# Optimization experiments

Hardware: AMD Instinct MI355X
Metric: run time of the kernel (lower is better)

Reference implementation:

```python
import jax, jax.numpy as jnp
import numpy as np

N = 50000      # nodes
E = 1600000    # edges (avg degree 32)
D_IN = 32
D_EF = 16
D_H = 64
D_MSG = 32
D_UP = 32


def setup_inputs() -> dict:
    key = jax.random.key(0)
    ks = jax.random.split(key, 10)
    s = 0.05
    return {
        "x": jax.random.normal(ks[0], (N, D_IN), dtype=jnp.float32),
        "degrees": jax.random.uniform(ks[1], (N, 1), dtype=jnp.float32),
        "edge_features": jax.random.normal(ks[2], (E, D_EF), dtype=jnp.float32),
        "W1m": jax.random.normal(ks[3], (2 * D_IN + D_EF, D_H), dtype=jnp.float32) * s,
        "b1m": jnp.zeros((D_H,), dtype=jnp.float32),
        "W2m": jax.random.normal(ks[4], (D_H, D_MSG), dtype=jnp.float32) * s,
        "b2m": jnp.zeros((D_MSG,), dtype=jnp.float32),
        "W1u": jax.random.normal(ks[5], (D_IN + D_MSG, D_H), dtype=jnp.float32) * s,
        "b1u": jnp.zeros((D_H,), dtype=jnp.float32),
        "W2u": jax.random.normal(ks[6], (D_H, D_UP), dtype=jnp.float32) * s,
        "b2u": jnp.zeros((D_UP,), dtype=jnp.float32),
        "edge_index": jax.random.randint(ks[7], (2, E), 0, N, dtype=jnp.int64),
    }


def mlp2(h, W1, b1, W2, b2):
    return jax.nn.relu(h @ W1 + b1) @ W2 + b2


def reference(x, degrees, edge_features, W1m, b1m, W2m, b2m, W1u, b1u, W2u, b2u, edge_index):
    # flow = 'source_to_target': select=1 -> i = targets = edge_index[1],
    # j = sources = edge_index[0]; sparse.sum over dim 0 aggregates per target.
    src = edge_index[0]
    dst = edge_index[1]
    x_i = x[dst]                                  # [E, D_IN] target features
    x_j = x[src]                                  # [E, D_IN] source features
    msg_in = jnp.concatenate([x_i, x_j, edge_features], axis=-1)  # [E, 2*D_IN+D_EF]
    msgs = mlp2(msg_in, W1m, b1m, W2m, b2m)       # [E, D_MSG]
    agg = jax.ops.segment_sum(msgs, dst, num_segments=x.shape[0])  # [N, D_MSG]
    upd_in = jnp.concatenate([x, agg], axis=-1)   # [N, D_IN+D_MSG]
    return mlp2(upd_in, W1u, b1u, W2u, b2u)       # [N, D_UP]
```

## Files before the change

### kernel.cpp

```cpp
#include <hip/hip_runtime.h>
#include <hip/hip_bf16.h>

#define D_IN  32
#define D_EF  16
#define D_H   64
#define D_MSG 32
#define D_UP  32

typedef __fp16 v2h __attribute__((ext_vector_type(2)));

__device__ __forceinline__ unsigned bf16pair(float a, float b) {
    unsigned ua = __float_as_uint(a);
    ua = (ua + 0x7fffu + ((ua >> 16) & 1u)) >> 16;
    unsigned ub = __float_as_uint(b);
    ub = (ub + 0x7fffu + ((ub >> 16) & 1u)) >> 16;
    return ua | (ub << 16);
}
__device__ __forceinline__ float bf_lo(unsigned u) { return __uint_as_float(u << 16); }
__device__ __forceinline__ float bf_hi(unsigned u) { return __uint_as_float(u & 0xffff0000u); }

__global__ __launch_bounds__(256) void prep_kernel(
    const float* __restrict__ x,
    const float* __restrict__ W1m,
    const float* __restrict__ b1m,
    const int*   __restrict__ ei,
    float* __restrict__ P1,
    unsigned short* __restrict__ P2b,
    int* __restrict__ deg,
    int* __restrict__ rank,
    v2h* __restrict__ W1Ep,
    int n_nodes, int n_edges, int NBn, int NBe)
{
    int b = blockIdx.x;

    if (b < NBn) {
        int i = b * 256 + threadIdx.x;
        if (i >= n_nodes) return;

        float xi[D_IN];
        const float4* xp = (const float4*)(x + (size_t)i * D_IN);
#pragma unroll
        for (int k4 = 0; k4 < D_IN / 4; ++k4) {
            float4 v = xp[k4];
            xi[4 * k4 + 0] = v.x; xi[4 * k4 + 1] = v.y;
            xi[4 * k4 + 2] = v.z; xi[4 * k4 + 3] = v.w;
        }
        {
            float acc[D_H];
#pragma unroll
            for (int j = 0; j < D_H; ++j) acc[j] = b1m[j];
            for (int k = 0; k < D_IN; ++k) {
                float xv = xi[k];
                const float* wr = W1m + (size_t)k * D_H;
#pragma unroll
                for (int j = 0; j < D_H; ++j) acc[j] += xv * wr[j];
            }
            float4* o = (float4*)(P1 + (size_t)i * D_H);
#pragma unroll
            for (int j4 = 0; j4 < D_H / 4; ++j4)
                o[j4] = make_float4(acc[4 * j4], acc[4 * j4 + 1],
                                    acc[4 * j4 + 2], acc[4 * j4 + 3]);
        }
        {
            float acc[D_H];
#pragma unroll
            for (int j = 0; j < D_H; ++j) acc[j] = 0.0f;
            for (int k = 0; k < D_IN; ++k) {
                float xv = xi[k];
                const float* wr = W1m + (size_t)(k + D_IN) * D_H;
#pragma unroll
                for (int j = 0; j < D_H; ++j) acc[j] += xv * wr[j];
            }
            uint4* o = (uint4*)(P2b + (size_t)i * D_H);
#pragma unroll
            for (int j8 = 0; j8 < D_H / 8; ++j8) {
                uint4 q;
                q.x = bf16pair(acc[8 * j8 + 0], acc[8 * j8 + 1]);
                q.y = bf16pair(acc[8 * j8 + 2], acc[8 * j8 + 3]);
                q.z = bf16pair(acc[8 * j8 + 4], acc[8 * j8 + 5]);
                q.w = bf16pair(acc[8 * j8 + 6], acc[8 * j8 + 7]);
                o[j8] = q;
            }
        }
    } else if (b < NBn + NBe) {
        int e = (b - NBn) * 256 + threadIdx.x;
        if (e < n_edges)
            rank[e] = atomicAdd(&deg[ei[n_edges + e]], 1);
    } else {
        int t = threadIdx.x;
        const float* W1E = W1m + (size_t)(2 * D_IN) * D_H;
        for (int idx = t; idx < 8 * D_H; idx += 256) {
            int kp = idx >> 6, c = idx & 63;
            W1Ep[idx] = __builtin_amdgcn_cvt_pkrtz(W1E[(2 * kp) * D_H + c],
                                                   W1E[(2 * kp + 1) * D_H + c]);
        }
    }
}

__global__ __launch_bounds__(256) void scan_partials_kernel(
    const int* __restrict__ deg, int* __restrict__ bsum, int n_nodes)
{
    int idx = blockIdx.x * 256 + threadIdx.x;
    int v = (idx < n_nodes) ? deg[idx] : 0;
#pragma unroll
    for (int o = 1; o < 64; o <<= 1) v += __shfl_xor(v, o, 64);
    __shared__ int ws[4];
    int lane = threadIdx.x & 63, w = threadIdx.x >> 6;
    if (lane == 0) ws[w] = v;
    __syncthreads();
    if (threadIdx.x == 0) bsum[blockIdx.x] = ws[0] + ws[1] + ws[2] + ws[3];
}

__global__ __launch_bounds__(256) void scan_blockoffs_kernel(
    const int* __restrict__ bsum, int* __restrict__ boffs, int nb)
{
    __shared__ int sdata[256];
    int t = threadIdx.x;
    sdata[t] = (t < nb) ? bsum[t] : 0;
    __syncthreads();
    for (int off = 1; off < 256; off <<= 1) {
        int u = (t >= off) ? sdata[t - off] : 0;
        __syncthreads();
        sdata[t] += u;
        __syncthreads();
    }
    if (t < nb) boffs[t] = (t > 0) ? sdata[t - 1] : 0;
}

__global__ __launch_bounds__(256) void scan_final_kernel(
    const int* __restrict__ deg, const int* __restrict__ boffs,
    int* __restrict__ offs, int n_nodes)
{
    __shared__ int sdata[256];
    int t = threadIdx.x;
    int idx = blockIdx.x * 256 + t;
    sdata[t] = (idx < n_nodes) ? deg[idx] : 0;
    __syncthreads();
    for (int off = 1; off < 256; off <<= 1) {
        int u = (t >= off) ? sdata[t - off] : 0;
        __syncthreads();
        sdata[t] += u;
        __syncthreads();
    }
    int excl = boffs[blockIdx.x] + ((t > 0) ? sdata[t - 1] : 0);
    if (idx < n_nodes) offs[idx] = excl;
}

__global__ __launch_bounds__(256) void scatter_kernel(
    const int* __restrict__ ei,
    const int* __restrict__ rank,
    const int* __restrict__ offs,
    int2* __restrict__ edges_sorted,
    int n_edges)
{
    int e = blockIdx.x * blockDim.x + threadIdx.x;
    if (e < n_edges) {
        int s = ei[e];
        int d = ei[n_edges + e];
        int pos = offs[d] + rank[e];
        edges_sorted[pos] = make_int2(e, s);
    }
}

__global__ __launch_bounds__(256, 6) void gather_kernel(
    const float* __restrict__ ef,
    const v2h*  __restrict__ W1Ep,
    const float* __restrict__ P1,
    const unsigned short* __restrict__ P2b,
    const int*  __restrict__ deg,
    const int*  __restrict__ offs,
    const int2* __restrict__ edges_sorted,
    float* __restrict__ hagg,
    int n_nodes)
{
    const int lane = threadIdx.x & 63;
    const int cg   = __builtin_amdgcn_readfirstlane((int)(threadIdx.x >> 6));
    const int g    = lane >> 4;
    const int t    = lane & 15;
    const int n    = blockIdx.x * 4 + g;
    if (n >= n_nodes) return;

    const int start = offs[n];
    const int end   = start + deg[n];

    float p1q[16];
    {
        const float4* pp = (const float4*)(P1 + (size_t)n * D_H + cg * 16);
#pragma unroll
        for (int q = 0; q < 4; ++q) {
            float4 v = pp[q];
            p1q[4 * q + 0] = v.x; p1q[4 * q + 1] = v.y;
            p1q[4 * q + 2] = v.z; p1q[4 * q + 3] = v.w;
        }
    }

    const v2h* wbase = W1Ep + 16 * cg;

    float hacc[16];
#pragma unroll
    for (int c = 0; c < 16; ++c) hacc[c] = 0.0f;

    for (int i = start + t; i < end; i += 16) {
        int2 es = edges_sorted[i];
        const float4* efp = (const float4*)(ef + (size_t)es.x * D_EF);
        float4 f0 = efp[0], f1 = efp[1], f2 = efp[2], f3 = efp[3];
        const uint4* p2u = (const uint4*)(P2b + (size_t)es.y * D_H + cg * 16);
        uint4 b0 = p2u[0], b1 = p2u[1];

        v2h efh[D_EF / 2];
        efh[0] = __builtin_amdgcn_cvt_pkrtz(f0.x, f0.y);
        efh[1] = __builtin_amdgcn_cvt_pkrtz(f0.z, f0.w);
        efh[2] = __builtin_amdgcn_cvt_pkrtz(f1.x, f1.y);
        efh[3] = __builtin_amdgcn_cvt_pkrtz(f1.z, f1.w);
        efh[4] = __builtin_amdgcn_cvt_pkrtz(f2.x, f2.y);
        efh[5] = __builtin_amdgcn_cvt_pkrtz(f2.z, f2.w);
        efh[6] = __builtin_amdgcn_cvt_pkrtz(f3.x, f3.y);
        efh[7] = __builtin_amdgcn_cvt_pkrtz(f3.z, f3.w);

#pragma unroll
        for (int jj = 0; jj < 2; ++jj) {
            uint4 b = jj ? b1 : b0;
            float h[8];
            h[0] = p1q[8 * jj + 0] + bf_lo(b.x);
            h[1] = p1q[8 * jj + 1] + bf_hi(b.x);
            h[2] = p1q[8 * jj + 2] + bf_lo(b.y);
            h[3] = p1q[8 * jj + 3] + bf_hi(b.y);
            h[4] = p1q[8 * jj + 4] + bf_lo(b.z);
            h[5] = p1q[8 * jj + 5] + bf_hi(b.z);
            h[6] = p1q[8 * jj + 6] + bf_lo(b.w);
            h[7] = p1q[8 * jj + 7] + bf_hi(b.w);

#pragma unroll
            for (int kp = 0; kp < D_EF / 2; ++kp) {
                const v2h* wr = wbase + kp * D_H + 8 * jj;
#pragma unroll
                for (int c8 = 0; c8 < 8; ++c8)
                    h[c8] = __builtin_amdgcn_fdot2(efh[kp], wr[c8], h[c8], false);
            }

#pragma unroll
            for (int c8 = 0; c8 < 8; ++c8) {
                float r = h[c8] > 0.0f ? h[c8] : 0.0f;
                hacc[8 * jj + c8] += r;
            }
        }
    }

    float r1[8];
    {
        const bool up = (t & 8) != 0;
#pragma unroll
        for (int c = 0; c < 8; ++c) {
            float lo = hacc[c]     + __shfl_xor(hacc[c],     8, 16);
            float hi = hacc[c + 8] + __shfl_xor(hacc[c + 8], 8, 16);
            r1[c] = up ? hi : lo;
        }
    }
    float r2[4];
    {
        const bool up = (t & 4) != 0;
#pragma unroll
        for (int c = 0; c < 4; ++c) {
            float lo = r1[c]     + __shfl_xor(r1[c],     4, 16);
            float hi = r1[c + 4] + __shfl_xor(r1[c + 4], 4, 16);
            r2[c] = up ? hi : lo;
        }
    }
    float r3[2];
    {
        const bool up = (t & 2) != 0;
#pragma unroll
        for (int c = 0; c < 2; ++c) {
            float lo = r2[c]     + __shfl_xor(r2[c],     2, 16);
            float hi = r2[c + 2] + __shfl_xor(r2[c + 2], 2, 16);
            r3[c] = up ? hi : lo;
        }
    }
    float r4;
    {
        const bool up = (t & 1) != 0;
        float lo = r3[0] + __shfl_xor(r3[0], 1, 16);
        float hi = r3[1] + __shfl_xor(r3[1], 1, 16);
        r4 = up ? hi : lo;
    }

    hagg[(size_t)n * D_H + cg * 16 + t] = r4;
}

__global__ __launch_bounds__(256) void node_upd_kernel(
    const float* __restrict__ x,
    const float* __restrict__ hagg,
    const int*   __restrict__ deg,
    const float* __restrict__ b2m,
    const float* __restrict__ W2m,
    const float* __restrict__ W1u,
    const float* __restrict__ b1u,
    const float* __restrict__ W2u,
    const float* __restrict__ b2u,
    float* __restrict__ out,
    int n_nodes)
{
    int i = blockIdx.x * blockDim.x + threadIdx.x;
    if (i >= n_nodes) return;

    float in[D_IN + D_MSG];
    const float4* xp = (const float4*)(x + (size_t)i * D_IN);
#pragma unroll
    for (int k4 = 0; k4 < D_IN / 4; ++k4) {
        float4 v = xp[k4];
        in[4 * k4 + 0] = v.x; in[4 * k4 + 1] = v.y;
        in[4 * k4 + 2] = v.z; in[4 * k4 + 3] = v.w;
    }

    float dc = (float)deg[i];
#pragma unroll
    for (int m = 0; m < D_MSG; ++m) in[D_IN + m] = dc * b2m[m];

    const float4* hp = (const float4*)(hagg + (size_t)i * D_H);
    for (int j4 = 0; j4 < D_H / 4; ++j4) {
        float4 v = hp[j4];
        const float* w0 = W2m + (size_t)(4 * j4 + 0) * D_MSG;
        const float* w1 = W2m + (size_t)(4 * j4 + 1) * D_MSG;
        const float* w2 = W2m + (size_t)(4 * j4 + 2) * D_MSG;
        const float* w3 = W2m + (size_t)(4 * j4 + 3) * D_MSG;
#pragma unroll
        for (int m = 0; m < D_MSG; ++m)
            in[D_IN + m] += v.x * w0[m] + v.y * w1[m] + v.z * w2[m] + v.w * w3[m];
    }

    float h[D_H];
#pragma unroll
    for (int j = 0; j < D_H; ++j) h[j] = b1u[j];
    for (int k = 0; k < D_IN + D_MSG; ++k) {
        float v = in[k];
        const float* wr = W1u + (size_t)k * D_H;
#pragma unroll
        for (int j = 0; j < D_H; ++j) h[j] += v * wr[j];
    }

    float o[D_UP];
#pragma unroll
    for (int m = 0; m < D_UP; ++m) o[m] = b2u[m];
    for (int j = 0; j < D_H; ++j) {
        float r = h[j] > 0.0f ? h[j] : 0.0f;
        const float* wr = W2u + (size_t)j * D_UP;
#pragma unroll
        for (int m = 0; m < D_UP; ++m) o[m] += r * wr[m];
    }

    float4* op = (float4*)(out + (size_t)i * D_UP);
#pragma unroll
    for (int m4 = 0; m4 < D_UP / 4; ++m4)
        op[m4] = make_float4(o[4 * m4], o[4 * m4 + 1], o[4 * m4 + 2], o[4 * m4 + 3]);
}

extern "C" void kernel_launch(void* const* d_in, const int* in_sizes, int n_in,
                              void* d_out, int out_size, void* d_ws, size_t ws_size,
                              hipStream_t stream) {
    const float* x    = (const float*)d_in[0];
    const float* ef   = (const float*)d_in[2];
    const float* W1m  = (const float*)d_in[3];
    const float* b1m  = (const float*)d_in[4];
    const float* W2m  = (const float*)d_in[5];
    const float* b2m  = (const float*)d_in[6];
    const float* W1u  = (const float*)d_in[7];
    const float* b1u  = (const float*)d_in[8];
    const float* W2u  = (const float*)d_in[9];
    const float* b2u  = (const float*)d_in[10];
    const int*   ei   = (const int*)d_in[11];

    const int n_nodes = in_sizes[0] / D_IN;
    const int n_edges = in_sizes[11] / 2;

    float* out = (float*)d_out;

    const int NBn = (n_nodes + 255) / 256;
    const int NBe = (n_edges + 255) / 256;

    float*          P1  = (float*)d_ws;
    unsigned short* P2b = (unsigned short*)(P1 + (size_t)n_nodes * D_H);
    int2* edges_sorted  = (int2*)(P2b + (size_t)n_nodes * D_H);
    int* deg    = (int*)(edges_sorted + n_edges);
    int* offs   = deg    + n_nodes;
    int* bsum   = offs   + n_nodes;
    int* boffs  = bsum   + NBn;
    v2h* W1Ep   = (v2h*)(boffs + NBn);
    int*   rank = (int*)(W1Ep + 8 * D_H);
    float* hagg = (float*)rank;

    hipMemsetAsync(deg, 0, (size_t)n_nodes * sizeof(int), stream);

    prep_kernel<<<NBn + NBe + 1, 256, 0, stream>>>(
        x, W1m, b1m, ei, P1, P2b, deg, rank, W1Ep,
        n_nodes, n_edges, NBn, NBe);

    scan_partials_kernel<<<NBn, 256, 0, stream>>>(deg, bsum, n_nodes);
    scan_blockoffs_kernel<<<1, 256, 0, stream>>>(bsum, boffs, NBn);
    scan_final_kernel<<<NBn, 256, 0, stream>>>(deg, boffs, offs, n_nodes);

    scatter_kernel<<<NBe, 256, 0, stream>>>(ei, rank, offs, edges_sorted, n_edges);

    {
        int grid = (n_nodes + 3) / 4;
        gather_kernel<<<grid, 256, 0, stream>>>(ef, W1Ep, P1, P2b,
                                                deg, offs, edges_sorted, hagg,
                                                n_nodes);
    }
    node_upd_kernel<<<NBn, 256, 0, stream>>>(x, hagg, deg, b2m, W2m,
                                             W1u, b1u, W2u, b2u, out, n_nodes);
}
```

Before: 450.0 us.

## Fuse prep, scan and scatter into one cooperative kernel with register-held edges

Replaces the prep, three scan and scatter launches with a single cooperative persistent kernel that uses grid.sync between phases. Edge src, dst and rank are kept in registers (up to MAXE per thread) so the scatter phase does not re-read edge_index or a rank array, and the sorted edge list is written with nontemporal 64-bit stores. The gather loop is also unrolled to process two edges per iteration, giving more independent loads in flight. This trades launch overhead and memory round-trips for grid-wide barrier cost and register pressure, and it relies on the cooperative grid being large enough to cover NBn blocks.

```diff
diff --git a/kernel.cpp b/kernel.cpp
--- a/kernel.cpp
+++ b/kernel.cpp
@@ -1,11 +1,16 @@
 #include <hip/hip_runtime.h>
 #include <hip/hip_bf16.h>
+#include <hip/hip_cooperative_groups.h>
+
+namespace cg = cooperative_groups;
 
 #define D_IN  32
 #define D_EF  16
 #define D_H   64
 #define D_MSG 32
 #define D_UP  32
+
+#define MAXE 7
 
 typedef __fp16 v2h __attribute__((ext_vector_type(2)));
 
@@ -19,7 +24,7 @@
 __device__ __forceinline__ float bf_lo(unsigned u) { return __uint_as_float(u << 16); }
 __device__ __forceinline__ float bf_hi(unsigned u) { return __uint_as_float(u & 0xffff0000u); }
 
-__global__ __launch_bounds__(256) void prep_kernel(
+__global__ __launch_bounds__(256, 4) void front_kernel(
     const float* __restrict__ x,
     const float* __restrict__ W1m,
     const float* __restrict__ b1m,
@@ -27,16 +32,31 @@
     float* __restrict__ P1,
     unsigned short* __restrict__ P2b,
     int* __restrict__ deg,
-    int* __restrict__ rank,
+    int* __restrict__ offs,
+    int* __restrict__ bsum,
+    int* __restrict__ boffs,
     v2h* __restrict__ W1Ep,
-    int n_nodes, int n_edges, int NBn, int NBe)
+    long long* __restrict__ edges_sorted,
+    int* __restrict__ rank_ovf,
+    int n_nodes, int n_edges, int NBn)
 {
-    int b = blockIdx.x;
-
-    if (b < NBn) {
-        int i = b * 256 + threadIdx.x;
-        if (i >= n_nodes) return;
-
+    cg::grid_group grid = cg::this_grid();
+    const int t   = threadIdx.x;
+    const int tid = blockIdx.x * 256 + t;
+    const int nth = gridDim.x * 256;
+
+    __shared__ int sdata[256];
+
+    if (blockIdx.x == 0) {
+        const float* W1E = W1m + (size_t)(2 * D_IN) * D_H;
+        for (int idx = t; idx < 8 * D_H; idx += 256) {
+            int kp = idx >> 6, c = idx & 63;
+            W1Ep[idx] = __builtin_amdgcn_cvt_pkrtz(W1E[(2 * kp) * D_H + c],
+                                                   W1E[(2 * kp + 1) * D_H + c]);
+        }
+    }
+
+    for (int i = tid; i < n_nodes; i += nth) {
         float xi[D_IN];
         const float4* xp = (const float4*)(x + (size_t)i * D_IN);
 #pragma unroll
@@ -45,35 +65,35 @@
             xi[4 * k4 + 0] = v.x; xi[4 * k4 + 1] = v.y;
             xi[4 * k4 + 2] = v.z; xi[4 * k4 + 3] = v.w;
         }
-        {
-            float acc[D_H];
-#pragma unroll
-            for (int j = 0; j < D_H; ++j) acc[j] = b1m[j];
+        for (int half = 0; half < 2; ++half) {
+            float acc[32];
+#pragma unroll
+            for (int j = 0; j < 32; ++j) acc[j] = b1m[half * 32 + j];
             for (int k = 0; k < D_IN; ++k) {
                 float xv = xi[k];
-                const float* wr = W1m + (size_t)k * D_H;
-#pragma unroll
-                for (int j = 0; j < D_H; ++j) acc[j] += xv * wr[j];
-            }
-            float4* o = (float4*)(P1 + (size_t)i * D_H);
-#pragma unroll
-            for (int j4 = 0; j4 < D_H / 4; ++j4)
+                const float* wr = W1m + (size_t)k * D_H + half * 32;
+#pragma unroll
+                for (int j = 0; j < 32; ++j) acc[j] += xv * wr[j];
+            }
+            float4* o = (float4*)(P1 + (size_t)i * D_H + half * 32);
+#pragma unroll
+            for (int j4 = 0; j4 < 8; ++j4)
                 o[j4] = make_float4(acc[4 * j4], acc[4 * j4 + 1],
                                     acc[4 * j4 + 2], acc[4 * j4 + 3]);
         }
-        {
-            float acc[D_H];
-#pragma unroll
-            for (int j = 0; j < D_H; ++j) acc[j] = 0.0f;
+        for (int half = 0; half < 2; ++half) {
+            float acc[32];
+#pragma unroll
+            for (int j = 0; j < 32; ++j) acc[j] = 0.0f;
             for (int k = 0; k < D_IN; ++k) {
                 float xv = xi[k];
-                const float* wr = W1m + (size_t)(k + D_IN) * D_H;
-#pragma unroll
-                for (int j = 0; j < D_H; ++j) acc[j] += xv * wr[j];
-            }
-            uint4* o = (uint4*)(P2b + (size_t)i * D_H);
-#pragma unroll
-            for (int j8 = 0; j8 < D_H / 8; ++j8) {
+                const float* wr = W1m + (size_t)(k + D_IN) * D_H + half * 32;
+#pragma unroll
+                for (int j = 0; j < 32; ++j) acc[j] += xv * wr[j];
+            }
+            uint4* o = (uint4*)(P2b + (size_t)i * D_H + half * 32);
+#pragma unroll
+            for (int j8 = 0; j8 < 4; ++j8) {
                 uint4 q;
                 q.x = bf16pair(acc[8 * j8 + 0], acc[8 * j8 + 1]);
                 q.y = bf16pair(acc[8 * j8 + 2], acc[8 * j8 + 3]);
@@ -82,99 +102,97 @@
                 o[j8] = q;
             }
         }
-    } else if (b < NBn + NBe) {
-        int e = (b - NBn) * 256 + threadIdx.x;
-        if (e < n_edges)
-            rank[e] = atomicAdd(&deg[ei[n_edges + e]], 1);
-    } else {
-        int t = threadIdx.x;
-        const float* W1E = W1m + (size_t)(2 * D_IN) * D_H;
-        for (int idx = t; idx < 8 * D_H; idx += 256) {
-            int kp = idx >> 6, c = idx & 63;
-            W1Ep[idx] = __builtin_amdgcn_cvt_pkrtz(W1E[(2 * kp) * D_H + c],
-                                                   W1E[(2 * kp + 1) * D_H + c]);
-        }
-    }
-}
-
-__global__ __launch_bounds__(256) void scan_partials_kernel(
-    const int* __restrict__ deg, int* __restrict__ bsum, int n_nodes)
-{
-    int idx = blockIdx.x * 256 + threadIdx.x;
-    int v = (idx < n_nodes) ? deg[idx] : 0;
-#pragma unroll
-    for (int o = 1; o < 64; o <<= 1) v += __shfl_xor(v, o, 64);
-    __shared__ int ws[4];
-    int lane = threadIdx.x & 63, w = threadIdx.x >> 6;
-    if (lane == 0) ws[w] = v;
-    __syncthreads();
-    if (threadIdx.x == 0) bsum[blockIdx.x] = ws[0] + ws[1] + ws[2] + ws[3];
-}
-
-__global__ __launch_bounds__(256) void scan_blockoffs_kernel(
-    const int* __restrict__ bsum, int* __restrict__ boffs, int nb)
-{
-    __shared__ int sdata[256];
-    int t = threadIdx.x;
-    sdata[t] = (t < nb) ? bsum[t] : 0;
-    __syncthreads();
-    for (int off = 1; off < 256; off <<= 1) {
-        int u = (t >= off) ? sdata[t - off] : 0;
+    }
+
+    int esrc[MAXE], edst[MAXE], ernk[MAXE];
+#pragma unroll
+    for (int q = 0; q < MAXE; ++q) {
+        int e = tid + q * nth;
+        esrc[q] = 0; edst[q] = 0; ernk[q] = 0;
+        if (e < n_edges) {
+            esrc[q] = ei[e];
+            edst[q] = ei[n_edges + e];
+            ernk[q] = atomicAdd(&deg[edst[q]], 1);
+        }
+    }
+    for (int e = tid + MAXE * nth; e < n_edges; e += nth)
+        rank_ovf[e] = atomicAdd(&deg[ei[n_edges + e]], 1);
+
+    grid.sync();
+
+    {
+        int b = blockIdx.x;
+        if (b < NBn) {
+            int idx = b * 256 + t;
+            sdata[t] = (idx < n_nodes) ? deg[idx] : 0;
+            __syncthreads();
+            for (int off = 1; off < 256; off <<= 1) {
+                int u = (t >= off) ? sdata[t - off] : 0;
+                __syncthreads();
+                sdata[t] += u;
+                __syncthreads();
+            }
+            if (t == 255) bsum[b] = sdata[255];
+            if (idx < n_nodes) offs[idx] = (t > 0) ? sdata[t - 1] : 0;
+        }
+    }
+    grid.sync();
+
+    if (blockIdx.x == 0) {
+        sdata[t] = (t < NBn) ? bsum[t] : 0;
         __syncthreads();
-        sdata[t] += u;
-        __syncthreads();
-    }
-    if (t < nb) boffs[t] = (t > 0) ? sdata[t - 1] : 0;
-}
-
-__global__ __launch_bounds__(256) void scan_final_kernel(
-    const int* __restrict__ deg, const int* __restrict__ boffs,
-    int* __restrict__ offs, int n_nodes)
-{
-    __shared__ int sdata[256];
-    int t = threadIdx.x;
-    int idx = blockIdx.x * 256 + t;
-    sdata[t] = (idx < n_nodes) ? deg[idx] : 0;
-    __syncthreads();
-    for (int off = 1; off < 256; off <<= 1) {
-        int u = (t >= off) ? sdata[t - off] : 0;
-        __syncthreads();
-        sdata[t] += u;
-        __syncthreads();
-    }
-    int excl = boffs[blockIdx.x] + ((t > 0) ? sdata[t - 1] : 0);
-    if (idx < n_nodes) offs[idx] = excl;
-}
-
-__global__ __launch_bounds__(256) void scatter_kernel(
-    const int* __restrict__ ei,
-    const int* __restrict__ rank,
-    const int* __restrict__ offs,
-    int2* __restrict__ edges_sorted,
-    int n_edges)
-{
-    int e = blockIdx.x * blockDim.x + threadIdx.x;
-    if (e < n_edges) {
+        for (int off = 1; off < 256; off <<= 1) {
+            int u = (t >= off) ? sdata[t - off] : 0;
+            __syncthreads();
+            sdata[t] += u;
+            __syncthreads();
+        }
+        if (t < NBn) boffs[t] = (t > 0) ? sdata[t - 1] : 0;
+    }
+    grid.sync();
+
+    {
+        int b = blockIdx.x;
+        if (b > 0 && b < NBn) {
+            int idx = b * 256 + t;
+            if (idx < n_nodes) offs[idx] += boffs[b];
+        }
+    }
+    grid.sync();
+
+#pragma unroll
+    for (int q = 0; q < MAXE; ++q) {
+        int e = tid + q * nth;
+        if (e < n_edges) {
+            int pos = offs[edst[q]] + ernk[q];
+            long long v = (long long)((unsigned long long)(unsigned)esrc[q] << 32)
+                        | (unsigned long long)(unsigned)e;
+            __builtin_nontemporal_store(v, &edges_sorted[pos]);
+        }
+    }
+    for (int e = tid + MAXE * nth; e < n_edges; e += nth) {
         int s = ei[e];
         int d = ei[n_edges + e];
-        int pos = offs[d] + rank[e];
-        edges_sorted[pos] = make_int2(e, s);
+        int pos = offs[d] + rank_ovf[e];
+        long long v = (long long)((unsigned long long)(unsigned)s << 32)
+                    | (unsigned long long)(unsigned)e;
+        edges_sorted[pos] = v;
     }
 }
 
-__global__ __launch_bounds__(256, 6) void gather_kernel(
+__global__ __launch_bounds__(256) void gather_kernel(
     const float* __restrict__ ef,
     const v2h*  __restrict__ W1Ep,
     const float* __restrict__ P1,
     const unsigned short* __restrict__ P2b,
     const int*  __restrict__ deg,
     const int*  __restrict__ offs,
-    const int2* __restrict__ edges_sorted,
+    const long long* __restrict__ edges_sorted,
     float* __restrict__ hagg,
     int n_nodes)
 {
     const int lane = threadIdx.x & 63;
-    const int cg   = __builtin_amdgcn_readfirstlane((int)(threadIdx.x >> 6));
+    const int cq   = __builtin_amdgcn_readfirstlane((int)(threadIdx.x >> 6));
     const int g    = lane >> 4;
     const int t    = lane & 15;
     const int n    = blockIdx.x * 4 + g;
@@ -185,7 +203,7 @@
 
     float p1q[16];
     {
-        const float4* pp = (const float4*)(P1 + (size_t)n * D_H + cg * 16);
+        const float4* pp = (const float4*)(P1 + (size_t)n * D_H + cq * 16);
 #pragma unroll
         for (int q = 0; q < 4; ++q) {
             float4 v = pp[q];
@@ -194,54 +212,95 @@
         }
     }
 
-    const v2h* wbase = W1Ep + 16 * cg;
+    const v2h* wbase = W1Ep + 16 * cq;
 
     float hacc[16];
 #pragma unroll
     for (int c = 0; c < 16; ++c) hacc[c] = 0.0f;
 
-    for (int i = start + t; i < end; i += 16) {
-        int2 es = edges_sorted[i];
-        const float4* efp = (const float4*)(ef + (size_t)es.x * D_EF);
-        float4 f0 = efp[0], f1 = efp[1], f2 = efp[2], f3 = efp[3];
-        const uint4* p2u = (const uint4*)(P2b + (size_t)es.y * D_H + cg * 16);
-        uint4 b0 = p2u[0], b1 = p2u[1];
-
-        v2h efh[D_EF / 2];
-        efh[0] = __builtin_amdgcn_cvt_pkrtz(f0.x, f0.y);
-        efh[1] = __builtin_amdgcn_cvt_pkrtz(f0.z, f0.w);
-        efh[2] = __builtin_amdgcn_cvt_pkrtz(f1.x, f1.y);
-        efh[3] = __builtin_amdgcn_cvt_pkrtz(f1.z, f1.w);
-        efh[4] = __builtin_amdgcn_cvt_pkrtz(f2.x, f2.y);
-        efh[5] = __builtin_amdgcn_cvt_pkrtz(f2.z, f2.w);
-        efh[6] = __builtin_amdgcn_cvt_pkrtz(f3.x, f3.y);
-        efh[7] = __builtin_amdgcn_cvt_pkrtz(f3.z, f3.w);
+    for (int i = start + t; i < end; i += 32) {
+        const int  iB = i + 16;
+        const bool hB = iB < end;
+        long long eA = edges_sorted[i];
+        long long eB = edges_sorted[hB ? iB : i];
+        int exA = (int)eA, syA = (int)(eA >> 32);
+        int exB = (int)eB, syB = (int)(eB >> 32);
+
+        const float4* fpA = (const float4*)(ef + (size_t)(unsigned)exA * D_EF);
+        const float4* fpB = (const float4*)(ef + (size_t)(unsigned)exB * D_EF);
+        float4 A0 = fpA[0], A1 = fpA[1], A2 = fpA[2], A3 = fpA[3];
+        float4 B0 = fpB[0], B1 = fpB[1], B2 = fpB[2], B3 = fpB[3];
+        const uint4* pA = (const uint4*)(P2b + (size_t)(unsigned)syA * D_H + cq * 16);
+        const uint4* pB = (const uint4*)(P2b + (size_t)(unsigned)syB * D_H + cq * 16);
+        uint4 a0 = pA[0], a1 = pA[1];
+        uint4 b0 = pB[0], b1 = pB[1];
+
+        v2h ehA[8], ehB[8];
+        ehA[0] = __builtin_amdgcn_cvt_pkrtz(A0.x, A0.y);
+        ehA[1] = __builtin_amdgcn_cvt_pkrtz(A0.z, A0.w);
+        ehA[2] = __builtin_amdgcn_cvt_pkrtz(A1.x, A1.y);
+        ehA[3] = __builtin_amdgcn_cvt_pkrtz(A1.z, A1.w);
+        ehA[4] = __builtin_amdgcn_cvt_pkrtz(A2.x, A2.y);
+        ehA[5] = __builtin_amdgcn_cvt_pkrtz(A2.z, A2.w);
+        ehA[6] = __builtin_amdgcn_cvt_pkrtz(A3.x, A3.y);
+        ehA[7] = __builtin_amdgcn_cvt_pkrtz(A3.z, A3.w);
+        ehB[0] = __builtin_amdgcn_cvt_pkrtz(B0.x, B0.y);
+        ehB[1] = __builtin_amdgcn_cvt_pkrtz(B0.z, B0.w);
+        ehB[2] = __builtin_amdgcn_cvt_pkrtz(B1.x, B1.y);
+        ehB[3] = __builtin_amdgcn_cvt_pkrtz(B1.z, B1.w);
+        ehB[4] = __builtin_amdgcn_cvt_pkrtz(B2.x, B2.y);
+        ehB[5] = __builtin_amdgcn_cvt_pkrtz(B2.z, B2.w);
+        ehB[6] = __builtin_amdgcn_cvt_pkrtz(B3.x, B3.y);
+        ehB[7] = __builtin_amdgcn_cvt_pkrtz(B3.z, B3.w);
 
 #pragma unroll
         for (int jj = 0; jj < 2; ++jj) {
-            uint4 b = jj ? b1 : b0;
+            uint4 bb = jj ? a1 : a0;
             float h[8];
-            h[0] = p1q[8 * jj + 0] + bf_lo(b.x);
-            h[1] = p1q[8 * jj + 1] + bf_hi(b.x);
-            h[2] = p1q[8 * jj + 2] + bf_lo(b.y);
-            h[3] = p1q[8 * jj + 3] + bf_hi(b.y);
-            h[4] = p1q[8 * jj + 4] + bf_lo(b.z);
-            h[5] = p1q[8 * jj + 5] + bf_hi(b.z);
-            h[6] = p1q[8 * jj + 6] + bf_lo(b.w);
-            h[7] = p1q[8 * jj + 7] + bf_hi(b.w);
-
+            h[0] = p1q[8 * jj + 0] + bf_lo(bb.x);
+            h[1] = p1q[8 * jj + 1] + bf_hi(bb.x);
+            h[2] = p1q[8 * jj + 2] + bf_lo(bb.y);
+            h[3] = p1q[8 * jj + 3] + bf_hi(bb.y);
+            h[4] = p1q[8 * jj + 4] + bf_lo(bb.z);
+            h[5] = p1q[8 * jj + 5] + bf_hi(bb.z);
+            h[6] = p1q[8 * jj + 6] + bf_lo(bb.w);
+            h[7] = p1q[8 * jj + 7] + bf_hi(bb.w);
 #pragma unroll
             for (int kp = 0; kp < D_EF / 2; ++kp) {
                 const v2h* wr = wbase + kp * D_H + 8 * jj;
 #pragma unroll
                 for (int c8 = 0; c8 < 8; ++c8)
-                    h[c8] = __builtin_amdgcn_fdot2(efh[kp], wr[c8], h[c8], false);
-            }
-
+                    h[c8] = __builtin_amdgcn_fdot2(ehA[kp], wr[c8], h[c8], false);
+            }
 #pragma unroll
             for (int c8 = 0; c8 < 8; ++c8) {
                 float r = h[c8] > 0.0f ? h[c8] : 0.0f;
                 hacc[8 * jj + c8] += r;
+            }
+        }
+#pragma unroll
+        for (int jj = 0; jj < 2; ++jj) {
+            uint4 bb = jj ? b1 : b0;
+            float h[8];
+            h[0] = p1q[8 * jj + 0] + bf_lo(bb.x);
+            h[1] = p1q[8 * jj + 1] + bf_hi(bb.x);
+            h[2] = p1q[8 * jj + 2] + bf_lo(bb.y);
+            h[3] = p1q[8 * jj + 3] + bf_hi(bb.y);
+            h[4] = p1q[8 * jj + 4] + bf_lo(bb.z);
+            h[5] = p1q[8 * jj + 5] + bf_hi(bb.z);
+            h[6] = p1q[8 * jj + 6] + bf_lo(bb.w);
+            h[7] = p1q[8 * jj + 7] + bf_hi(bb.w);
+#pragma unroll
+            for (int kp = 0; kp < D_EF / 2; ++kp) {
+                const v2h* wr = wbase + kp * D_H + 8 * jj;
+#pragma unroll
+                for (int c8 = 0; c8 < 8; ++c8)
+                    h[c8] = __builtin_amdgcn_fdot2(ehB[kp], wr[c8], h[c8], false);
+            }
+#pragma unroll
+            for (int c8 = 0; c8 < 8; ++c8) {
+                float r = h[c8] > 0.0f ? h[c8] : 0.0f;
+                hacc[8 * jj + c8] += hB ? r : 0.0f;
             }
         }
     }
@@ -284,7 +343,7 @@
         r4 = up ? hi : lo;
     }
 
-    hagg[(size_t)n * D_H + cg * 16 + t] = r4;
+    hagg[(size_t)n * D_H + cq * 16 + t] = r4;
 }
 
 __global__ __launch_bounds__(256) void node_upd_kernel(
@@ -375,30 +434,45 @@
     float* out = (float*)d_out;
 
     const int NBn = (n_nodes + 255) / 256;
-    const int NBe = (n_edges + 255) / 256;
 
     float*          P1  = (float*)d_ws;
     unsigned short* P2b = (unsigned short*)(P1 + (size_t)n_nodes * D_H);
-    int2* edges_sorted  = (int2*)(P2b + (size_t)n_nodes * D_H);
+    long long* edges_sorted = (long long*)(P2b + (size_t)n_nodes * D_H);
     int* deg    = (int*)(edges_sorted + n_edges);
     int* offs   = deg    + n_nodes;
     int* bsum   = offs   + n_nodes;
-    int* boffs  = bsum   + NBn;
-    v2h* W1Ep   = (v2h*)(boffs + NBn);
-    int*   rank = (int*)(W1Ep + 8 * D_H);
-    float* hagg = (float*)rank;
+    int* boffs  = bsum   + 256;
+    v2h* W1Ep   = (v2h*)(boffs + 256);
+    int* rank_ovf = (int*)(W1Ep + 8 * D_H);
+    float* hagg   = (float*)rank_ovf;
+
+    static int s_G = 0;
+    if (s_G == 0) {
+        hipDeviceProp_t prop;
+        hipGetDeviceProperties(&prop, 0);
+        int nbpc = 0;
+        hipOccupancyMaxActiveBlocksPerMultiprocessor(&nbpc, front_kernel, 256, 0);
+        if (nbpc < 1) nbpc = 1;
+        if (nbpc > 4) nbpc = 4;
+        int g = prop.multiProcessorCount * nbpc;
+        if (g > 2048) g = 2048;
+        if (g < NBn) g = NBn;
+        s_G = g;
+    }
 
     hipMemsetAsync(deg, 0, (size_t)n_nodes * sizeof(int), stream);
 
-    prep_kernel<<<NBn + NBe + 1, 256, 0, stream>>>(
-        x, W1m, b1m, ei, P1, P2b, deg, rank, W1Ep,
-        n_nodes, n_edges, NBn, NBe);
-
-    scan_partials_kernel<<<NBn, 256, 0, stream>>>(deg, bsum, n_nodes);
-    scan_blockoffs_kernel<<<1, 256, 0, stream>>>(bsum, boffs, NBn);
-    scan_final_kernel<<<NBn, 256, 0, stream>>>(deg, boffs, offs, n_nodes);
-
-    scatter_kernel<<<NBe, 256, 0, stream>>>(ei, rank, offs, edges_sorted, n_edges);
+    {
+        int ne = n_edges, nn = n_nodes, nb = NBn;
+        void* args[] = {
+            (void*)&x, (void*)&W1m, (void*)&b1m, (void*)&ei,
+            (void*)&P1, (void*)&P2b, (void*)&deg, (void*)&offs,
+            (void*)&bsum, (void*)&boffs, (void*)&W1Ep, (void*)&edges_sorted,
+            (void*)&rank_ovf, (void*)&nn, (void*)&ne, (void*)&nb
+        };
+        hipLaunchCooperativeKernel(front_kernel, dim3(s_G), dim3(256),
+                                   args, 0, stream);
+    }
 
     {
         int grid = (n_nodes + 3) / 4;
```

After: 825.1 us. +83.3%, slower.

## Stage edge features in shared memory per node and merge scan kernels

Applied to the files above, without the earlier changes.

The gather kernel now loads each node's first 64 sorted edges once per block into LDS: the source index plus edge features packed to fp16. Previously each of the four column-group wavefronts re-read edge_sorted and the 64-byte edge features from global memory, so this removes three redundant loads per edge. Edges beyond 64 fall back to the old path. The separate block-offset scan kernel is folded into the final scan, with every block re-scanning the block sums, and the occupancy hint of 6 in launch_bounds is dropped. The cost is a block-wide barrier and LDS usage that may reduce occupancy.

```diff
diff --git a/kernel.cpp b/kernel.cpp
--- a/kernel.cpp
+++ b/kernel.cpp
@@ -7,7 +7,10 @@
 #define D_MSG 32
 #define D_UP  32
 
+#define MAXS 64
+
 typedef __fp16 v2h __attribute__((ext_vector_type(2)));
+typedef float v4f __attribute__((ext_vector_type(4)));
 
 __device__ __forceinline__ unsigned bf16pair(float a, float b) {
     unsigned ua = __float_as_uint(a);
@@ -97,7 +100,7 @@
     }
 }
 
-__global__ __launch_bounds__(256) void scan_partials_kernel(
+__global__ __launch_bounds__(256) void scan_reduce_kernel(
     const int* __restrict__ deg, int* __restrict__ bsum, int n_nodes)
 {
     int idx = blockIdx.x * 256 + threadIdx.x;
@@ -111,28 +114,24 @@
     if (threadIdx.x == 0) bsum[blockIdx.x] = ws[0] + ws[1] + ws[2] + ws[3];
 }
 
-__global__ __launch_bounds__(256) void scan_blockoffs_kernel(
-    const int* __restrict__ bsum, int* __restrict__ boffs, int nb)
-{
+__global__ __launch_bounds__(256) void scan_final_kernel(
+    const int* __restrict__ deg, const int* __restrict__ bsum,
+    int* __restrict__ offs, int n_nodes, int nb)
+{
+    __shared__ int sb[256];
     __shared__ int sdata[256];
     int t = threadIdx.x;
-    sdata[t] = (t < nb) ? bsum[t] : 0;
+
+    sb[t] = (t < nb) ? bsum[t] : 0;
     __syncthreads();
     for (int off = 1; off < 256; off <<= 1) {
-        int u = (t >= off) ? sdata[t - off] : 0;
+        int u = (t >= off) ? sb[t - off] : 0;
         __syncthreads();
-        sdata[t] += u;
+        sb[t] += u;
         __syncthreads();
     }
-    if (t < nb) boffs[t] = (t > 0) ? sdata[t - 1] : 0;
-}
-
-__global__ __launch_bounds__(256) void scan_final_kernel(
-    const int* __restrict__ deg, const int* __restrict__ boffs,
-    int* __restrict__ offs, int n_nodes)
-{
-    __shared__ int sdata[256];
-    int t = threadIdx.x;
+    int base = (blockIdx.x > 0) ? sb[blockIdx.x - 1] : 0;
+
     int idx = blockIdx.x * 256 + t;
     sdata[t] = (idx < n_nodes) ? deg[idx] : 0;
     __syncthreads();
@@ -142,8 +141,7 @@
         sdata[t] += u;
         __syncthreads();
     }
-    int excl = boffs[blockIdx.x] + ((t > 0) ? sdata[t - 1] : 0);
-    if (idx < n_nodes) offs[idx] = excl;
+    if (idx < n_nodes) offs[idx] = base + ((t > 0) ? sdata[t - 1] : 0);
 }
 
 __global__ __launch_bounds__(256) void scatter_kernel(
@@ -162,7 +160,7 @@
     }
 }
 
-__global__ __launch_bounds__(256, 6) void gather_kernel(
+__global__ __launch_bounds__(256) void gather_kernel(
     const float* __restrict__ ef,
     const v2h*  __restrict__ W1Ep,
     const float* __restrict__ P1,
@@ -173,19 +171,56 @@
     float* __restrict__ hagg,
     int n_nodes)
 {
-    const int lane = threadIdx.x & 63;
-    const int cg   = __builtin_amdgcn_readfirstlane((int)(threadIdx.x >> 6));
+    __shared__ v2h efs[4][MAXS][10];
+    __shared__ int ssrc[4][MAXS];
+
+    const int tid = threadIdx.x;
+
+    {
+        const int sg = tid >> 6;
+        const int ss = tid & 63;
+        const int nS = blockIdx.x * 4 + sg;
+        int cntS = 0, offS = 0;
+        if (nS < n_nodes) {
+            int d = deg[nS];
+            offS = offs[nS];
+            cntS = d < MAXS ? d : MAXS;
+        }
+        if (ss < cntS) {
+            int2 es = edges_sorted[offS + ss];
+            ssrc[sg][ss] = es.y;
+            const v4f* efp = (const v4f*)(ef + (size_t)(unsigned)es.x * D_EF);
+            v4f f0 = __builtin_nontemporal_load(&efp[0]);
+            v4f f1 = __builtin_nontemporal_load(&efp[1]);
+            v4f f2 = __builtin_nontemporal_load(&efp[2]);
+            v4f f3 = __builtin_nontemporal_load(&efp[3]);
+            efs[sg][ss][0] = __builtin_amdgcn_cvt_pkrtz(f0.x, f0.y);
+            efs[sg][ss][1] = __builtin_amdgcn_cvt_pkrtz(f0.z, f0.w);
+            efs[sg][ss][2] = __builtin_amdgcn_cvt_pkrtz(f1.x, f1.y);
+            efs[sg][ss][3] = __builtin_amdgcn_cvt_pkrtz(f1.z, f1.w);
+            efs[sg][ss][4] = __builtin_amdgcn_cvt_pkrtz(f2.x, f2.y);
+            efs[sg][ss][5] = __builtin_amdgcn_cvt_pkrtz(f2.z, f2.w);
+            efs[sg][ss][6] = __builtin_amdgcn_cvt_pkrtz(f3.x, f3.y);
+            efs[sg][ss][7] = __builtin_amdgcn_cvt_pkrtz(f3.z, f3.w);
+        }
+    }
+    __syncthreads();
+
+    const int lane = tid & 63;
+    const int cq   = __builtin_amdgcn_readfirstlane((int)(tid >> 6));
     const int g    = lane >> 4;
     const int t    = lane & 15;
     const int n    = blockIdx.x * 4 + g;
-    if (n >= n_nodes) return;
-
-    const int start = offs[n];
-    const int end   = start + deg[n];
+
+    int degC = 0, offC = 0;
+    if (n < n_nodes) { degC = deg[n]; offC = offs[n]; }
+    const int cnt = degC < MAXS ? degC : MAXS;
 
     float p1q[16];
-    {
-        const float4* pp = (const float4*)(P1 + (size_t)n * D_H + cg * 16);
+#pragma unroll
+    for (int q = 0; q < 16; ++q) p1q[q] = 0.0f;
+    if (n < n_nodes) {
+        const float4* pp = (const float4*)(P1 + (size_t)n * D_H + cq * 16);
 #pragma unroll
         for (int q = 0; q < 4; ++q) {
             float4 v = pp[q];
@@ -194,20 +229,56 @@
         }
     }
 
-    const v2h* wbase = W1Ep + 16 * cg;
+    const v2h* wbase = W1Ep + 16 * cq;
 
     float hacc[16];
 #pragma unroll
     for (int c = 0; c < 16; ++c) hacc[c] = 0.0f;
 
-    for (int i = start + t; i < end; i += 16) {
-        int2 es = edges_sorted[i];
-        const float4* efp = (const float4*)(ef + (size_t)es.x * D_EF);
+    for (int i = t; i < cnt; i += 16) {
+        int s = ssrc[g][i];
+        const uint4* p2u = (const uint4*)(P2b + (size_t)(unsigned)s * D_H + cq * 16);
+        uint4 b0 = p2u[0], b1 = p2u[1];
+
+        v2h efh[8];
+#pragma unroll
+        for (int k = 0; k < 8; ++k) efh[k] = efs[g][i][k];
+
+#pragma unroll
+        for (int jj = 0; jj < 2; ++jj) {
+            uint4 bb = jj ? b1 : b0;
+            float h[8];
+            h[0] = p1q[8 * jj + 0] + bf_lo(bb.x);
+            h[1] = p1q[8 * jj + 1] + bf_hi(bb.x);
+            h[2] = p1q[8 * jj + 2] + bf_lo(bb.y);
+            h[3] = p1q[8 * jj + 3] + bf_hi(bb.y);
+            h[4] = p1q[8 * jj + 4] + bf_lo(bb.z);
+            h[5] = p1q[8 * jj + 5] + bf_hi(bb.z);
+            h[6] = p1q[8 * jj + 6] + bf_lo(bb.w);
+            h[7] = p1q[8 * jj + 7] + bf_hi(bb.w);
+#pragma unroll
+            for (int kp = 0; kp < D_EF / 2; ++kp) {
+                const v2h* wr = wbase + kp * D_H + 8 * jj;
+#pragma unroll
+                for (int c8 = 0; c8 < 8; ++c8)
+                    h[c8] = __builtin_amdgcn_fdot2(efh[kp], wr[c8], h[c8], false);
+            }
+#pragma unroll
+            for (int c8 = 0; c8 < 8; ++c8) {
+                float r = h[c8] > 0.0f ? h[c8] : 0.0f;
+                hacc[8 * jj + c8] += r;
+            }
+        }
+    }
+
+    for (int i = MAXS + t; i < degC; i += 16) {
+        int2 es = edges_sorted[offC + i];
+        const float4* efp = (const float4*)(ef + (size_t)(unsigned)es.x * D_EF);
         float4 f0 = efp[0], f1 = efp[1], f2 = efp[2], f3 = efp[3];
-        const uint4* p2u = (const uint4*)(P2b + (size_t)es.y * D_H + cg * 16);
+        const uint4* p2u = (const uint4*)(P2b + (size_t)(unsigned)es.y * D_H + cq * 16);
         uint4 b0 = p2u[0], b1 = p2u[1];
 
-        v2h efh[D_EF / 2];
+        v2h efh[8];
         efh[0] = __builtin_amdgcn_cvt_pkrtz(f0.x, f0.y);
         efh[1] = __builtin_amdgcn_cvt_pkrtz(f0.z, f0.w);
         efh[2] = __builtin_amdgcn_cvt_pkrtz(f1.x, f1.y);
@@ -219,17 +290,16 @@
 
 #pragma unroll
         for (int jj = 0; jj < 2; ++jj) {
-            uint4 b = jj ? b1 : b0;
+            uint4 bb = jj ? b1 : b0;
             float h[8];
-            h[0] = p1q[8 * jj + 0] + bf_lo(b.x);
-            h[1] = p1q[8 * jj + 1] + bf_hi(b.x);
-            h[2] = p1q[8 * jj + 2] + bf_lo(b.y);
-            h[3] = p1q[8 * jj + 3] + bf_hi(b.y);
-            h[4] = p1q[8 * jj + 4] + bf_lo(b.z);
-            h[5] = p1q[8 * jj + 5] + bf_hi(b.z);
-            h[6] = p1q[8 * jj + 6] + bf_lo(b.w);
-            h[7] = p1q[8 * jj + 7] + bf_hi(b.w);
-
+            h[0] = p1q[8 * jj + 0] + bf_lo(bb.x);
+            h[1] = p1q[8 * jj + 1] + bf_hi(bb.x);
+            h[2] = p1q[8 * jj + 2] + bf_lo(bb.y);
+            h[3] = p1q[8 * jj + 3] + bf_hi(bb.y);
+            h[4] = p1q[8 * jj + 4] + bf_lo(bb.z);
+            h[5] = p1q[8 * jj + 5] + bf_hi(bb.z);
+            h[6] = p1q[8 * jj + 6] + bf_lo(bb.w);
+            h[7] = p1q[8 * jj + 7] + bf_hi(bb.w);
 #pragma unroll
             for (int kp = 0; kp < D_EF / 2; ++kp) {
                 const v2h* wr = wbase + kp * D_H + 8 * jj;
@@ -237,7 +307,6 @@
                 for (int c8 = 0; c8 < 8; ++c8)
                     h[c8] = __builtin_amdgcn_fdot2(efh[kp], wr[c8], h[c8], false);
             }
-
 #pragma unroll
             for (int c8 = 0; c8 < 8; ++c8) {
                 float r = h[c8] > 0.0f ? h[c8] : 0.0f;
@@ -284,7 +353,8 @@
         r4 = up ? hi : lo;
     }
 
-    hagg[(size_t)n * D_H + cg * 16 + t] = r4;
+    if (n < n_nodes)
+        hagg[(size_t)n * D_H + cq * 16 + t] = r4;
 }
 
 __global__ __launch_bounds__(256) void node_upd_kernel(
@@ -383,9 +453,8 @@
     int* deg    = (int*)(edges_sorted + n_edges);
     int* offs   = deg    + n_nodes;
     int* bsum   = offs   + n_nodes;
-    int* boffs  = bsum   + NBn;
-    v2h* W1Ep   = (v2h*)(boffs + NBn);
-    int*   rank = (int*)(W1Ep + 8 * D_H);
+    v2h* W1Ep   = (v2h*)(bsum + 256);
+    int* rank   = (int*)(W1Ep + 8 * D_H);
     float* hagg = (float*)rank;
 
     hipMemsetAsync(deg, 0, (size_t)n_nodes * sizeof(int), stream);
@@ -394,9 +463,8 @@
         x, W1m, b1m, ei, P1, P2b, deg, rank, W1Ep,
         n_nodes, n_edges, NBn, NBe);
 
-    scan_partials_kernel<<<NBn, 256, 0, stream>>>(deg, bsum, n_nodes);
-    scan_blockoffs_kernel<<<1, 256, 0, stream>>>(bsum, boffs, NBn);
-    scan_final_kernel<<<NBn, 256, 0, stream>>>(deg, boffs, offs, n_nodes);
+    scan_reduce_kernel<<<NBn, 256, 0, stream>>>(deg, bsum, n_nodes);
+    scan_final_kernel<<<NBn, 256, 0, stream>>>(deg, bsum, offs, n_nodes, NBn);
 
     scatter_kernel<<<NBe, 256, 0, stream>>>(ei, rank, offs, edges_sorted, n_edges);
 
```

Result: slower. 534.1 us (+18.7%).

## Map one wavefront per node with lane-per-hidden-channel and merge scan kernels

Applied to the files above, without the earlier changes.

The gather kernel now assigns one 64-lane wavefront per destination node, with each lane owning one hidden channel. Lanes walk the node's edges serially with a one-edge prefetch of the sorted edge index, which removes the cross-lane shuffle reduction and the 16-channel register tiles. The block-offset scan is folded into the final scan kernel, so each block rescans the block sums redundantly and one launch is dropped. The trade-off is that every lane of a wave now loads the same edge-feature row (broadcast) and the edges of a node are processed sequentially, with less edge-level parallelism per node.

```diff
diff --git a/kernel.cpp b/kernel.cpp
--- a/kernel.cpp
+++ b/kernel.cpp
@@ -97,7 +97,7 @@
     }
 }
 
-__global__ __launch_bounds__(256) void scan_partials_kernel(
+__global__ __launch_bounds__(256) void scan_reduce_kernel(
     const int* __restrict__ deg, int* __restrict__ bsum, int n_nodes)
 {
     int idx = blockIdx.x * 256 + threadIdx.x;
@@ -111,28 +111,24 @@
     if (threadIdx.x == 0) bsum[blockIdx.x] = ws[0] + ws[1] + ws[2] + ws[3];
 }
 
-__global__ __launch_bounds__(256) void scan_blockoffs_kernel(
-    const int* __restrict__ bsum, int* __restrict__ boffs, int nb)
-{
+__global__ __launch_bounds__(256) void scan_final_kernel(
+    const int* __restrict__ deg, const int* __restrict__ bsum,
+    int* __restrict__ offs, int n_nodes, int nb)
+{
+    __shared__ int sb[256];
     __shared__ int sdata[256];
     int t = threadIdx.x;
-    sdata[t] = (t < nb) ? bsum[t] : 0;
+
+    sb[t] = (t < nb) ? bsum[t] : 0;
     __syncthreads();
     for (int off = 1; off < 256; off <<= 1) {
-        int u = (t >= off) ? sdata[t - off] : 0;
+        int u = (t >= off) ? sb[t - off] : 0;
         __syncthreads();
-        sdata[t] += u;
+        sb[t] += u;
         __syncthreads();
     }
-    if (t < nb) boffs[t] = (t > 0) ? sdata[t - 1] : 0;
-}
-
-__global__ __launch_bounds__(256) void scan_final_kernel(
-    const int* __restrict__ deg, const int* __restrict__ boffs,
-    int* __restrict__ offs, int n_nodes)
-{
-    __shared__ int sdata[256];
-    int t = threadIdx.x;
+    int base = (blockIdx.x > 0) ? sb[blockIdx.x - 1] : 0;
+
     int idx = blockIdx.x * 256 + t;
     sdata[t] = (idx < n_nodes) ? deg[idx] : 0;
     __syncthreads();
@@ -142,8 +138,7 @@
         sdata[t] += u;
         __syncthreads();
     }
-    int excl = boffs[blockIdx.x] + ((t > 0) ? sdata[t - 1] : 0);
-    if (idx < n_nodes) offs[idx] = excl;
+    if (idx < n_nodes) offs[idx] = base + ((t > 0) ? sdata[t - 1] : 0);
 }
 
 __global__ __launch_bounds__(256) void scatter_kernel(
@@ -162,7 +157,7 @@
     }
 }
 
-__global__ __launch_bounds__(256, 6) void gather_kernel(
+__global__ __launch_bounds__(256) void gather_kernel(
     const float* __restrict__ ef,
     const v2h*  __restrict__ W1Ep,
     const float* __restrict__ P1,
@@ -174,117 +169,55 @@
     int n_nodes)
 {
     const int lane = threadIdx.x & 63;
-    const int cg   = __builtin_amdgcn_readfirstlane((int)(threadIdx.x >> 6));
-    const int g    = lane >> 4;
-    const int t    = lane & 15;
-    const int n    = blockIdx.x * 4 + g;
+    const int n    = blockIdx.x * 4 + (threadIdx.x >> 6);
     if (n >= n_nodes) return;
 
     const int start = offs[n];
     const int end   = start + deg[n];
 
-    float p1q[16];
-    {
-        const float4* pp = (const float4*)(P1 + (size_t)n * D_H + cg * 16);
-#pragma unroll
-        for (int q = 0; q < 4; ++q) {
-            float4 v = pp[q];
-            p1q[4 * q + 0] = v.x; p1q[4 * q + 1] = v.y;
-            p1q[4 * q + 2] = v.z; p1q[4 * q + 3] = v.w;
-        }
-    }
-
-    const v2h* wbase = W1Ep + 16 * cg;
-
-    float hacc[16];
-#pragma unroll
-    for (int c = 0; c < 16; ++c) hacc[c] = 0.0f;
-
-    for (int i = start + t; i < end; i += 16) {
-        int2 es = edges_sorted[i];
-        const float4* efp = (const float4*)(ef + (size_t)es.x * D_EF);
+    v2h wcol[8];
+#pragma unroll
+    for (int kp = 0; kp < 8; ++kp) wcol[kp] = W1Ep[kp * D_H + lane];
+    const float p1 = P1[(size_t)n * D_H + lane];
+
+    float hacc = 0.0f;
+
+    int i = start;
+    int2 esC;
+    if (i < end) esC = edges_sorted[i];
+    while (i < end) {
+        const int inx = i + 1;
+        int2 esN = edges_sorted[inx < end ? inx : i];
+
+        const float4* efp = (const float4*)(ef + (size_t)(unsigned)esC.x * D_EF);
         float4 f0 = efp[0], f1 = efp[1], f2 = efp[2], f3 = efp[3];
-        const uint4* p2u = (const uint4*)(P2b + (size_t)es.y * D_H + cg * 16);
-        uint4 b0 = p2u[0], b1 = p2u[1];
-
-        v2h efh[D_EF / 2];
-        efh[0] = __builtin_amdgcn_cvt_pkrtz(f0.x, f0.y);
-        efh[1] = __builtin_amdgcn_cvt_pkrtz(f0.z, f0.w);
-        efh[2] = __builtin_amdgcn_cvt_pkrtz(f1.x, f1.y);
-        efh[3] = __builtin_amdgcn_cvt_pkrtz(f1.z, f1.w);
-        efh[4] = __builtin_amdgcn_cvt_pkrtz(f2.x, f2.y);
-        efh[5] = __builtin_amdgcn_cvt_pkrtz(f2.z, f2.w);
-        efh[6] = __builtin_amdgcn_cvt_pkrtz(f3.x, f3.y);
-        efh[7] = __builtin_amdgcn_cvt_pkrtz(f3.z, f3.w);
-
-#pragma unroll
-        for (int jj = 0; jj < 2; ++jj) {
-            uint4 b = jj ? b1 : b0;
-            float h[8];
-            h[0] = p1q[8 * jj + 0] + bf_lo(b.x);
-            h[1] = p1q[8 * jj + 1] + bf_hi(b.x);
-            h[2] = p1q[8 * jj + 2] + bf_lo(b.y);
-            h[3] = p1q[8 * jj + 3] + bf_hi(b.y);
-            h[4] = p1q[8 * jj + 4] + bf_lo(b.z);
-            h[5] = p1q[8 * jj + 5] + bf_hi(b.z);
-            h[6] = p1q[8 * jj + 6] + bf_lo(b.w);
-            h[7] = p1q[8 * jj + 7] + bf_hi(b.w);
-
-#pragma unroll
-            for (int kp = 0; kp < D_EF / 2; ++kp) {
-                const v2h* wr = wbase + kp * D_H + 8 * jj;
-#pragma unroll
-                for (int c8 = 0; c8 < 8; ++c8)
-                    h[c8] = __builtin_amdgcn_fdot2(efh[kp], wr[c8], h[c8], false);
-            }
-
-#pragma unroll
-            for (int c8 = 0; c8 < 8; ++c8) {
-                float r = h[c8] > 0.0f ? h[c8] : 0.0f;
-                hacc[8 * jj + c8] += r;
-            }
-        }
-    }
-
-    float r1[8];
-    {
-        const bool up = (t & 8) != 0;
-#pragma unroll
-        for (int c = 0; c < 8; ++c) {
-            float lo = hacc[c]     + __shfl_xor(hacc[c],     8, 16);
-            float hi = hacc[c + 8] + __shfl_xor(hacc[c + 8], 8, 16);
-            r1[c] = up ? hi : lo;
-        }
-    }
-    float r2[4];
-    {
-        const bool up = (t & 4) != 0;
-#pragma unroll
-        for (int c = 0; c < 4; ++c) {
-            float lo = r1[c]     + __shfl_xor(r1[c],     4, 16);
-            float hi = r1[c + 4] + __shfl_xor(r1[c + 4], 4, 16);
-            r2[c] = up ? hi : lo;
-        }
-    }
-    float r3[2];
-    {
-        const bool up = (t & 2) != 0;
-#pragma unroll
-        for (int c = 0; c < 2; ++c) {
-            float lo = r2[c]     + __shfl_xor(r2[c],     2, 16);
-            float hi = r2[c + 2] + __shfl_xor(r2[c + 2], 2, 16);
-            r3[c] = up ? hi : lo;
-        }
-    }
-    float r4;
-    {
-        const bool up = (t & 1) != 0;
-        float lo = r3[0] + __shfl_xor(r3[0], 1, 16);
-        float hi = r3[1] + __shfl_xor(r3[1], 1, 16);
-        r4 = up ? hi : lo;
-    }
-
-    hagg[(size_t)n * D_H + cg * 16 + t] = r4;
+        unsigned p2 = P2b[(size_t)(unsigned)esC.y * D_H + lane];
+
+        v2h e0 = __builtin_amdgcn_cvt_pkrtz(f0.x, f0.y);
+        v2h e1 = __builtin_amdgcn_cvt_pkrtz(f0.z, f0.w);
+        v2h e2 = __builtin_amdgcn_cvt_pkrtz(f1.x, f1.y);
+        v2h e3 = __builtin_amdgcn_cvt_pkrtz(f1.z, f1.w);
+        v2h e4 = __builtin_amdgcn_cvt_pkrtz(f2.x, f2.y);
+        v2h e5 = __builtin_amdgcn_cvt_pkrtz(f2.z, f2.w);
+        v2h e6 = __builtin_amdgcn_cvt_pkrtz(f3.x, f3.y);
+        v2h e7 = __builtin_amdgcn_cvt_pkrtz(f3.z, f3.w);
+
+        float h = p1 + __uint_as_float(p2 << 16);
+        h = __builtin_amdgcn_fdot2(e0, wcol[0], h, false);
+        h = __builtin_amdgcn_fdot2(e1, wcol[1], h, false);
+        h = __builtin_amdgcn_fdot2(e2, wcol[2], h, false);
+        h = __builtin_amdgcn_fdot2(e3, wcol[3], h, false);
+        h = __builtin_amdgcn_fdot2(e4, wcol[4], h, false);
+        h = __builtin_amdgcn_fdot2(e5, wcol[5], h, false);
+        h = __builtin_amdgcn_fdot2(e6, wcol[6], h, false);
+        h = __builtin_amdgcn_fdot2(e7, wcol[7], h, false);
+        hacc += (h > 0.0f ? h : 0.0f);
+
+        esC = esN;
+        i = inx;
+    }
+
+    hagg[(size_t)n * D_H + lane] = hacc;
 }
 
 __global__ __launch_bounds__(256) void node_upd_kernel(
@@ -383,9 +316,8 @@
     int* deg    = (int*)(edges_sorted + n_edges);
     int* offs   = deg    + n_nodes;
     int* bsum   = offs   + n_nodes;
-    int* boffs  = bsum   + NBn;
-    v2h* W1Ep   = (v2h*)(boffs + NBn);
-    int*   rank = (int*)(W1Ep + 8 * D_H);
+    v2h* W1Ep   = (v2h*)(bsum + 256);
+    int* rank   = (int*)(W1Ep + 8 * D_H);
     float* hagg = (float*)rank;
 
     hipMemsetAsync(deg, 0, (size_t)n_nodes * sizeof(int), stream);
@@ -394,9 +326,8 @@
         x, W1m, b1m, ei, P1, P2b, deg, rank, W1Ep,
         n_nodes, n_edges, NBn, NBe);
 
-    scan_partials_kernel<<<NBn, 256, 0, stream>>>(deg, bsum, n_nodes);
-    scan_blockoffs_kernel<<<1, 256, 0, stream>>>(bsum, boffs, NBn);
-    scan_final_kernel<<<NBn, 256, 0, stream>>>(deg, boffs, offs, n_nodes);
+    scan_reduce_kernel<<<NBn, 256, 0, stream>>>(deg, bsum, n_nodes);
+    scan_final_kernel<<<NBn, 256, 0, stream>>>(deg, bsum, offs, n_nodes, NBn);
 
     scatter_kernel<<<NBe, 256, 0, stream>>>(ei, rank, offs, edges_sorted, n_edges);
 
```

Result: slower. 622.2 us (+38.3%).
